# Optimization experiments

Hardware: AMD Instinct MI355X
Metric: run time of the kernel (lower is better)

## Reference

```python
import jax, jax.numpy as jnp
import numpy as np

N_NODES = 100000
N_EDGES = 1600000
IN_CH = 128
HEADS = 4
OUT_CH = 32


def setup_inputs() -> dict:
    key = jax.random.key(0)
    k = jax.random.split(key, 6)
    x = jax.random.normal(k[0], (N_NODES, IN_CH), dtype=jnp.float32)
    edge_index = jax.random.randint(k[1], (2, N_EDGES), 0, N_NODES, dtype=jnp.int64)
    edge_weight = jax.random.uniform(k[2], (N_EDGES,), dtype=jnp.float32)
    # torch Linear weight layout: (out_features, in_features) = (heads*out_ch, in_ch)
    W = jax.random.normal(k[3], (HEADS * OUT_CH, IN_CH), dtype=jnp.float32) * (1.0 / np.sqrt(IN_CH))
    a_src = jax.random.normal(k[4], (1, HEADS, OUT_CH), dtype=jnp.float32) * 0.1
    a_dst = jax.random.normal(k[5], (1, HEADS, OUT_CH), dtype=jnp.float32) * 0.1
    return {"x": x, "edge_index": edge_index, "edge_weight": edge_weight,
            "W": W, "a_src": a_src, "a_dst": a_dst}


def reference(x, edge_index, edge_weight, W, a_src, a_dst):
    N = x.shape[0]
    H, C = a_src.shape[1], a_src.shape[2]
    # linear projection then reshape to (N, H, C)
    h = (x @ W.T).reshape(N, H, C)
    src, dst = edge_index[0], edge_index[1]
    # per-node attention logits (node-level, then gathered -> same math as
    # (h[src]*a_src).sum(-1), computed once per node instead of per edge)
    s_src = jnp.sum(h * a_src, axis=-1)  # (N, H)
    s_dst = jnp.sum(h * a_dst, axis=-1)  # (N, H)
    alpha = jax.nn.leaky_relu(s_src[src] + s_dst[dst], negative_slope=0.2)  # (E, H)
    alpha = alpha * edge_weight[:, None]
    # segment softmax over dst; torch scatter_reduce amax with include_self=True
    # includes the zero init, so max is taken vs. 0 via zeros init
    amax = jnp.zeros((N, H), dtype=alpha.dtype).at[dst].max(alpha)
    alpha = jnp.exp(alpha - amax[dst])
    asum = jnp.zeros((N, H), dtype=alpha.dtype).at[dst].add(alpha)
    alpha = alpha / (asum[dst] + 1e-8)  # (E, H)
    # weighted scatter-add aggregation
    out = jnp.zeros((N, H, C), dtype=h.dtype).at[dst].add(h[src] * alpha[:, :, None])
    # concat=True
    return out.reshape(N, H * C)
```

## Files before the change

### kernel.cpp

```cpp
#include <hip/hip_runtime.h>

#define N_NODES 100000
#define N_EDGES 1600000
#define NBKT 391
#define BKT_SLACK 5120
#define EPB 4096
#define BINA_BLOCKS ((N_EDGES + EPB - 1) / EPB)

typedef __attribute__((ext_vector_type(8))) short short8;
typedef __attribute__((ext_vector_type(4))) float f32x4;

__device__ __forceinline__ unsigned short f2bf(float f) {
    unsigned u = __float_as_uint(f);
    u = u + 0x7fffu + ((u >> 16) & 1u);
    return (unsigned short)(u >> 16);
}
__device__ __forceinline__ float bf2f(unsigned short h) {
    return __uint_as_float((unsigned)h << 16);
}

__global__ __launch_bounds__(256) void proj_kernel(
    const float* __restrict__ x, const float* __restrict__ W,
    const float* __restrict__ a_src, const float* __restrict__ a_dst,
    unsigned short* __restrict__ hout, float* __restrict__ s_src,
    float* __restrict__ s_dst)
{
    __shared__ char smem[16384];
    char* xh = smem;
    char* xl = smem + 8192;
    const int t = threadIdx.x;
    const int br = blockIdx.x * 32;
    const int wave = t >> 6, lane = t & 63;
    const int lr = lane & 15, q = lane >> 4;

    short8 wh[2][4], wl[2][4];
#pragma unroll
    for (int ct = 0; ct < 2; ++ct) {
#pragma unroll
        for (int ks = 0; ks < 4; ++ks) {
            int o = wave * 32 + ct * 16 + lr;
            int k0 = (ks * 4 + q) * 8;
            float4 v0 = *(const float4*)&W[o * 128 + k0];
            float4 v1 = *(const float4*)&W[o * 128 + k0 + 4];
            float vv[8] = {v0.x, v0.y, v0.z, v0.w, v1.x, v1.y, v1.z, v1.w};
            short8 h8, l8;
#pragma unroll
            for (int j = 0; j < 8; ++j) {
                unsigned short hi = f2bf(vv[j]);
                h8[j] = (short)hi;
                l8[j] = (short)f2bf(vv[j] - bf2f(hi));
            }
            wh[ct][ks] = h8;
            wl[ct][ks] = l8;
        }
    }

    {
        int row = t >> 3;
        size_t gb = (size_t)(br + row) * 128;
#pragma unroll
        for (int i = 0; i < 4; ++i) {
            int k = ((t & 7) * 4 + i) * 4;
            float4 v = *(const float4*)&x[gb + k];
            ushort4 hi, lo;
            hi.x = f2bf(v.x); lo.x = f2bf(v.x - bf2f(hi.x));
            hi.y = f2bf(v.y); lo.y = f2bf(v.y - bf2f(hi.y));
            hi.z = f2bf(v.z); lo.z = f2bf(v.z - bf2f(hi.z));
            hi.w = f2bf(v.w); lo.w = f2bf(v.w - bf2f(hi.w));
            int byt = row * 256 + (((k >> 3) ^ (row & 7)) * 16) + (k & 7) * 2;
            *(ushort4*)(xh + byt) = hi;
            *(ushort4*)(xl + byt) = lo;
        }
    }
    __syncthreads();

    f32x4 acc[2][2] = {};

#pragma unroll
    for (int ks = 0; ks < 4; ++ks) {
        int sl = ((ks * 4 + q) ^ (lr & 7)) * 16;
        int a0o = lr * 256 + sl, a1o = (16 + lr) * 256 + sl;
        short8 ah0 = *(const short8*)(xh + a0o);
        short8 ah1 = *(const short8*)(xh + a1o);
        short8 al0 = *(const short8*)(xl + a0o);
        short8 al1 = *(const short8*)(xl + a1o);
        acc[0][0] = __builtin_amdgcn_mfma_f32_16x16x32_bf16(ah0, wh[0][ks], acc[0][0], 0, 0, 0);
        acc[0][1] = __builtin_amdgcn_mfma_f32_16x16x32_bf16(ah0, wh[1][ks], acc[0][1], 0, 0, 0);
        acc[1][0] = __builtin_amdgcn_mfma_f32_16x16x32_bf16(ah1, wh[0][ks], acc[1][0], 0, 0, 0);
        acc[1][1] = __builtin_amdgcn_mfma_f32_16x16x32_bf16(ah1, wh[1][ks], acc[1][1], 0, 0, 0);
        acc[0][0] = __builtin_amdgcn_mfma_f32_16x16x32_bf16(al0, wh[0][ks], acc[0][0], 0, 0, 0);
        acc[0][1] = __builtin_amdgcn_mfma_f32_16x16x32_bf16(al0, wh[1][ks], acc[0][1], 0, 0, 0);
        acc[1][0] = __builtin_amdgcn_mfma_f32_16x16x32_bf16(al1, wh[0][ks], acc[1][0], 0, 0, 0);
        acc[1][1] = __builtin_amdgcn_mfma_f32_16x16x32_bf16(al1, wh[1][ks], acc[1][1], 0, 0, 0);
        acc[0][0] = __builtin_amdgcn_mfma_f32_16x16x32_bf16(ah0, wl[0][ks], acc[0][0], 0, 0, 0);
        acc[0][1] = __builtin_amdgcn_mfma_f32_16x16x32_bf16(ah0, wl[1][ks], acc[0][1], 0, 0, 0);
        acc[1][0] = __builtin_amdgcn_mfma_f32_16x16x32_bf16(ah1, wl[0][ks], acc[1][0], 0, 0, 0);
        acc[1][1] = __builtin_amdgcn_mfma_f32_16x16x32_bf16(ah1, wl[1][ks], acc[1][1], 0, 0, 0);
    }

    float as0 = a_src[wave * 32 + lr], as1 = a_src[wave * 32 + 16 + lr];
    float ad0 = a_dst[wave * 32 + lr], ad1 = a_dst[wave * 32 + 16 + lr];
#pragma unroll
    for (int r = 0; r < 2; ++r) {
#pragma unroll
        for (int reg = 0; reg < 4; ++reg) {
            float ps = acc[r][0][reg] * as0 + acc[r][1][reg] * as1;
            float pd = acc[r][0][reg] * ad0 + acc[r][1][reg] * ad1;
            ps += __shfl_xor(ps, 1); ps += __shfl_xor(ps, 2);
            ps += __shfl_xor(ps, 4); ps += __shfl_xor(ps, 8);
            pd += __shfl_xor(pd, 1); pd += __shfl_xor(pd, 2);
            pd += __shfl_xor(pd, 4); pd += __shfl_xor(pd, 8);
            if (lr == 0) {
                int grow = br + r * 16 + q * 4 + reg;
                s_src[grow * 4 + wave] = ps;
                s_dst[grow * 4 + wave] = pd;
            }
        }
    }

    __syncthreads();
    unsigned short* hl = (unsigned short*)smem;
#pragma unroll
    for (int r = 0; r < 2; ++r)
#pragma unroll
        for (int c = 0; c < 2; ++c)
#pragma unroll
            for (int reg = 0; reg < 4; ++reg)
                hl[(r * 16 + q * 4 + reg) * 128 + wave * 32 + c * 16 + lr] =
                    f2bf(acc[r][c][reg]);
    __syncthreads();
    {
        int row = t >> 3, cb = (t & 7) * 16;
        uint4 v0 = *(uint4*)&hl[row * 128 + cb];
        uint4 v1 = *(uint4*)&hl[row * 128 + cb + 8];
        *(uint4*)&hout[(size_t)(br + row) * 128 + cb] = v0;
        *(uint4*)&hout[(size_t)(br + row) * 128 + cb + 8] = v1;
    }
}

__global__ __launch_bounds__(256) void binA_kernel(
    const int* __restrict__ ei, const float* __restrict__ ew,
    int* __restrict__ gcur, uint2* __restrict__ ebin)
{
    __shared__ int hist[NBKT];
    __shared__ int runbase[NBKT];
    const int t = threadIdx.x;
    const int base = blockIdx.x * EPB;
    for (int b = t; b < NBKT; b += 256) hist[b] = 0;
    __syncthreads();
#pragma unroll
    for (int i = 0; i < EPB / 256; ++i) {
        int e = base + i * 256 + t;
        if (e < N_EDGES) atomicAdd(&hist[ei[N_EDGES + e] >> 8], 1);
    }
    __syncthreads();
    for (int b = t; b < NBKT; b += 256) {
        int c = hist[b];
        runbase[b] = (c > 0) ? atomicAdd(&gcur[b], c) : 0;
        hist[b] = 0;
    }
    __syncthreads();
#pragma unroll
    for (int i = 0; i < EPB / 256; ++i) {
        int e = base + i * 256 + t;
        if (e >= N_EDGES) continue;
        int s = ei[e];
        int d = ei[N_EDGES + e];
        int b = d >> 8;
        int lpos = atomicAdd(&hist[b], 1);
        ebin[(size_t)b * BKT_SLACK + runbase[b] + lpos] =
            make_uint2((unsigned)s | ((unsigned)(d & 255) << 17),
                       __float_as_uint(ew[e]));
    }
}

__global__ __launch_bounds__(256) void binB_kernel(
    const uint2* __restrict__ ebin, const int* __restrict__ gcur,
    uint2* __restrict__ earr, int* __restrict__ rowp, int* __restrict__ deg)
{
    __shared__ int cnt[256];
    __shared__ int sc[256];
    __shared__ int cur[256];
    const int b = blockIdx.x;
    const int t = threadIdx.x;
    int acc = 0;
    for (int i = t; i < b; i += 256) acc += gcur[i];
    sc[t] = acc; __syncthreads();
    for (int off = 1; off < 256; off <<= 1) {
        int a = sc[t];
        int bb = (t >= off) ? sc[t - off] : 0;
        __syncthreads();
        sc[t] = a + bb;
        __syncthreads();
    }
    const int base = sc[255];
    __syncthreads();
    cnt[t] = 0;
    __syncthreads();
    const int count = gcur[b];
    const uint2* bp = ebin + (size_t)b * BKT_SLACK;
    for (int i = t; i < count; i += 256)
        atomicAdd(&cnt[(bp[i].x >> 17) & 255], 1);
    __syncthreads();
    int c = cnt[t];
    sc[t] = c; __syncthreads();
    for (int off = 1; off < 256; off <<= 1) {
        int a = sc[t];
        int bb = (t >= off) ? sc[t - off] : 0;
        __syncthreads();
        sc[t] = a + bb;
        __syncthreads();
    }
    int excl = sc[t] - c;
    int node = b * 256 + t;
    if (node < N_NODES) { rowp[node] = base + excl; deg[node] = c; }
    cur[t] = base + excl;
    __syncthreads();
    for (int i = t; i < count; i += 256) {
        uint2 rec = bp[i];
        int pos = atomicAdd(&cur[(rec.x >> 17) & 255], 1);
        earr[pos] = make_uint2(rec.x & 0x1FFFFu, rec.y);
    }
}

__global__ __launch_bounds__(256) void gather_kernel(
    const uint2* __restrict__ earr, const int* __restrict__ rowp,
    const int* __restrict__ deg, const float* __restrict__ s_src,
    const float* __restrict__ s_dst,
    const unsigned short* __restrict__ hbuf, float* __restrict__ out)
{
    __shared__ float lds_alpha[16][17][4];
    __shared__ int lds_src[16][17];
    const int ln = threadIdx.x >> 4;
    const int sub = threadIdx.x & 15;
    const int n = blockIdx.x * 16 + ln;
    const int start = rowp[n];
    const int dg = deg[n];
    const float4 sd = *(const float4*)&s_dst[n * 4];
    const int hd3 = sub >> 2;

    float ps0 = 0.f, ps1 = 0.f, ps2 = 0.f, ps3 = 0.f;
    float ac0 = 0.f, ac1 = 0.f, ac2 = 0.f, ac3 = 0.f;
    float ac4 = 0.f, ac5 = 0.f, ac6 = 0.f, ac7 = 0.f;

    for (int b0 = 0; b0 < dg; b0 += 16) {
        int nb = dg - b0; if (nb > 16) nb = 16;
        float a0 = 0.f, a1 = 0.f, a2 = 0.f, a3 = 0.f;
        int sid = 0;
        if (sub < nb) {
            uint2 rec = earr[start + b0 + sub];
            sid = (int)rec.x;
            float wgt = __uint_as_float(rec.y);
            float4 ss = *(const float4*)&s_src[sid * 4];
            float v;
            v = ss.x + sd.x; v = (v > 0.f ? v : 0.2f * v) * wgt; a0 = __expf(v);
            v = ss.y + sd.y; v = (v > 0.f ? v : 0.2f * v) * wgt; a1 = __expf(v);
            v = ss.z + sd.z; v = (v > 0.f ? v : 0.2f * v) * wgt; a2 = __expf(v);
            v = ss.w + sd.w; v = (v > 0.f ? v : 0.2f * v) * wgt; a3 = __expf(v);
            ps0 += a0; ps1 += a1; ps2 += a2; ps3 += a3;
        }
        *(float4*)&lds_alpha[ln][sub][0] = make_float4(a0, a1, a2, a3);
        lds_src[ln][sub] = sid;

        float co[16];
        uint4 hv[16];
#pragma unroll
        for (int e = 0; e < 16; ++e) {
            co[e] = lds_alpha[ln][e][hd3];
            int s = lds_src[ln][e];
            hv[e] = *(const uint4*)&hbuf[(size_t)s * 128 + sub * 8];
        }
#pragma unroll
        for (int e = 0; e < 16; ++e) {
            ac0 = fmaf(co[e], __uint_as_float(hv[e].x << 16), ac0);
            ac1 = fmaf(co[e], __uint_as_float(hv[e].x & 0xffff0000u), ac1);
            ac2 = fmaf(co[e], __uint_as_float(hv[e].y << 16), ac2);
            ac3 = fmaf(co[e], __uint_as_float(hv[e].y & 0xffff0000u), ac3);
            ac4 = fmaf(co[e], __uint_as_float(hv[e].z << 16), ac4);
            ac5 = fmaf(co[e], __uint_as_float(hv[e].z & 0xffff0000u), ac5);
            ac6 = fmaf(co[e], __uint_as_float(hv[e].w << 16), ac6);
            ac7 = fmaf(co[e], __uint_as_float(hv[e].w & 0xffff0000u), ac7);
        }
    }
#pragma unroll
    for (int off = 1; off < 16; off <<= 1) {
        ps0 += __shfl_xor(ps0, off);
        ps1 += __shfl_xor(ps1, off);
        ps2 += __shfl_xor(ps2, off);
        ps3 += __shfl_xor(ps3, off);
    }
    float sv = (hd3 & 2) ? ((hd3 & 1) ? ps3 : ps2) : ((hd3 & 1) ? ps1 : ps0);
    float inv = 1.f / (sv + 1e-8f);
    float4 o0 = {ac0 * inv, ac1 * inv, ac2 * inv, ac3 * inv};
    float4 o1 = {ac4 * inv, ac5 * inv, ac6 * inv, ac7 * inv};
    *(float4*)&out[(size_t)n * 128 + sub * 8] = o0;
    *(float4*)&out[(size_t)n * 128 + sub * 8 + 4] = o1;
}

extern "C" void kernel_launch(void* const* d_in, const int* in_sizes, int n_in,
                              void* d_out, int out_size, void* d_ws, size_t ws_size,
                              hipStream_t stream)
{
    const float* x     = (const float*)d_in[0];
    const int*   ei    = (const int*)d_in[1];
    const float* ew    = (const float*)d_in[2];
    const float* W     = (const float*)d_in[3];
    const float* a_src = (const float*)d_in[4];
    const float* a_dst = (const float*)d_in[5];
    float* out = (float*)d_out;
    char* ws = (char*)d_ws;

    unsigned short* hbuf = (unsigned short*)(ws);
    float* s_src = (float*)(ws + 25600000);
    float* s_dst = (float*)(ws + 27200000);
    int*   deg   = (int*)(ws + 28800000);
    int*   rowp  = (int*)(ws + 29200000);
    int*   gcur  = (int*)(ws + 29600000);
    uint2* earr  = (uint2*)(ws + 29669632);
    uint2* ebin  = (uint2*)(ws + 42469632);

    hipMemsetAsync(gcur, 0, 2048, stream);

    proj_kernel<<<N_NODES / 32, 256, 0, stream>>>(x, W, a_src, a_dst,
                                                  hbuf, s_src, s_dst);
    binA_kernel<<<BINA_BLOCKS, 256, 0, stream>>>(ei, ew, gcur, ebin);
    binB_kernel<<<NBKT, 256, 0, stream>>>(ebin, gcur, earr, rowp, deg);
    gather_kernel<<<N_NODES / 16, 256, 0, stream>>>(earr, rowp, deg, s_src, s_dst,
                                                    hbuf, out);
}
```

Measured before the change: 166.0 us.

## Merge projection and edge binning into one launch, double projection rows per block

The projection and first edge-binning pass are combined into a single kernel whose grid is split by block index, so the two independent stages run concurrently and one launch is removed. Each projection block now handles 64 rows instead of 32, with bounds checks added for the tail. This amortizes the per-block W split into high and low bf16 halves over more rows. Shared memory grows to about 33KB for every block, including binning blocks that need far less, which may reduce occupancy.

```diff
diff --git a/kernel.cpp b/kernel.cpp
--- a/kernel.cpp
+++ b/kernel.cpp
@@ -6,6 +6,7 @@
 #define BKT_SLACK 5120
 #define EPB 4096
 #define BINA_BLOCKS ((N_EDGES + EPB - 1) / EPB)
+#define PROJ_BLOCKS ((N_NODES + 63) / 64)
 
 typedef __attribute__((ext_vector_type(8))) short short8;
 typedef __attribute__((ext_vector_type(4))) float f32x4;
@@ -19,17 +20,53 @@
     return __uint_as_float((unsigned)h << 16);
 }
 
-__global__ __launch_bounds__(256) void proj_kernel(
+__global__ __launch_bounds__(256) void projbinA_kernel(
     const float* __restrict__ x, const float* __restrict__ W,
     const float* __restrict__ a_src, const float* __restrict__ a_dst,
     unsigned short* __restrict__ hout, float* __restrict__ s_src,
-    float* __restrict__ s_dst)
+    float* __restrict__ s_dst,
+    const int* __restrict__ ei, const float* __restrict__ ew,
+    int* __restrict__ gcur, uint2* __restrict__ ebin)
 {
-    __shared__ char smem[16384];
+    __shared__ char smem[33024];
+    const int t = threadIdx.x;
+
+    if (blockIdx.x >= PROJ_BLOCKS) {
+        int* hist    = (int*)smem;
+        int* runbase = (int*)(smem + 1664);
+        const int base = (blockIdx.x - PROJ_BLOCKS) * EPB;
+        for (int b = t; b < NBKT; b += 256) hist[b] = 0;
+        __syncthreads();
+#pragma unroll
+        for (int i = 0; i < EPB / 256; ++i) {
+            int e = base + i * 256 + t;
+            if (e < N_EDGES) atomicAdd(&hist[ei[N_EDGES + e] >> 8], 1);
+        }
+        __syncthreads();
+        for (int b = t; b < NBKT; b += 256) {
+            int c = hist[b];
+            runbase[b] = (c > 0) ? atomicAdd(&gcur[b], c) : 0;
+            hist[b] = 0;
+        }
+        __syncthreads();
+#pragma unroll
+        for (int i = 0; i < EPB / 256; ++i) {
+            int e = base + i * 256 + t;
+            if (e >= N_EDGES) continue;
+            int s = ei[e];
+            int d = ei[N_EDGES + e];
+            int b = d >> 8;
+            int lpos = atomicAdd(&hist[b], 1);
+            ebin[(size_t)b * BKT_SLACK + runbase[b] + lpos] =
+                make_uint2((unsigned)s | ((unsigned)(d & 255) << 17),
+                           __float_as_uint(ew[e]));
+        }
+        return;
+    }
+
     char* xh = smem;
-    char* xl = smem + 8192;
-    const int t = threadIdx.x;
-    const int br = blockIdx.x * 32;
+    char* xl = smem + 16384;
+    const int br = blockIdx.x * 64;
     const int wave = t >> 6, lane = t & 63;
     const int lr = lane & 15, q = lane >> 4;
 
@@ -56,12 +93,14 @@
     }
 
     {
-        int row = t >> 3;
-        size_t gb = (size_t)(br + row) * 128;
-#pragma unroll
-        for (int i = 0; i < 4; ++i) {
-            int k = ((t & 7) * 4 + i) * 4;
-            float4 v = *(const float4*)&x[gb + k];
+        int row = t >> 2;
+        int gr = br + row;
+        size_t gb = (size_t)gr * 128;
+#pragma unroll
+        for (int i = 0; i < 8; ++i) {
+            int k = (t & 3) * 32 + i * 4;
+            float4 v = (gr < N_NODES) ? *(const float4*)&x[gb + k]
+                                      : make_float4(0.f, 0.f, 0.f, 0.f);
             ushort4 hi, lo;
             hi.x = f2bf(v.x); lo.x = f2bf(v.x - bf2f(hi.x));
             hi.y = f2bf(v.y); lo.y = f2bf(v.y - bf2f(hi.y));
@@ -74,34 +113,29 @@
     }
     __syncthreads();
 
-    f32x4 acc[2][2] = {};
+    f32x4 acc[4][2] = {};
 
 #pragma unroll
     for (int ks = 0; ks < 4; ++ks) {
         int sl = ((ks * 4 + q) ^ (lr & 7)) * 16;
-        int a0o = lr * 256 + sl, a1o = (16 + lr) * 256 + sl;
-        short8 ah0 = *(const short8*)(xh + a0o);
-        short8 ah1 = *(const short8*)(xh + a1o);
-        short8 al0 = *(const short8*)(xl + a0o);
-        short8 al1 = *(const short8*)(xl + a1o);
-        acc[0][0] = __builtin_amdgcn_mfma_f32_16x16x32_bf16(ah0, wh[0][ks], acc[0][0], 0, 0, 0);
-        acc[0][1] = __builtin_amdgcn_mfma_f32_16x16x32_bf16(ah0, wh[1][ks], acc[0][1], 0, 0, 0);
-        acc[1][0] = __builtin_amdgcn_mfma_f32_16x16x32_bf16(ah1, wh[0][ks], acc[1][0], 0, 0, 0);
-        acc[1][1] = __builtin_amdgcn_mfma_f32_16x16x32_bf16(ah1, wh[1][ks], acc[1][1], 0, 0, 0);
-        acc[0][0] = __builtin_amdgcn_mfma_f32_16x16x32_bf16(al0, wh[0][ks], acc[0][0], 0, 0, 0);
-        acc[0][1] = __builtin_amdgcn_mfma_f32_16x16x32_bf16(al0, wh[1][ks], acc[0][1], 0, 0, 0);
-        acc[1][0] = __builtin_amdgcn_mfma_f32_16x16x32_bf16(al1, wh[0][ks], acc[1][0], 0, 0, 0);
-        acc[1][1] = __builtin_amdgcn_mfma_f32_16x16x32_bf16(al1, wh[1][ks], acc[1][1], 0, 0, 0);
-        acc[0][0] = __builtin_amdgcn_mfma_f32_16x16x32_bf16(ah0, wl[0][ks], acc[0][0], 0, 0, 0);
-        acc[0][1] = __builtin_amdgcn_mfma_f32_16x16x32_bf16(ah0, wl[1][ks], acc[0][1], 0, 0, 0);
-        acc[1][0] = __builtin_amdgcn_mfma_f32_16x16x32_bf16(ah1, wl[0][ks], acc[1][0], 0, 0, 0);
-        acc[1][1] = __builtin_amdgcn_mfma_f32_16x16x32_bf16(ah1, wl[1][ks], acc[1][1], 0, 0, 0);
+#pragma unroll
+        for (int r = 0; r < 4; ++r) {
+            int ao = (r * 16 + lr) * 256 + sl;
+            short8 ah = *(const short8*)(xh + ao);
+            short8 al = *(const short8*)(xl + ao);
+            acc[r][0] = __builtin_amdgcn_mfma_f32_16x16x32_bf16(ah, wh[0][ks], acc[r][0], 0, 0, 0);
+            acc[r][1] = __builtin_amdgcn_mfma_f32_16x16x32_bf16(ah, wh[1][ks], acc[r][1], 0, 0, 0);
+            acc[r][0] = __builtin_amdgcn_mfma_f32_16x16x32_bf16(al, wh[0][ks], acc[r][0], 0, 0, 0);
+            acc[r][1] = __builtin_amdgcn_mfma_f32_16x16x32_bf16(al, wh[1][ks], acc[r][1], 0, 0, 0);
+            acc[r][0] = __builtin_amdgcn_mfma_f32_16x16x32_bf16(ah, wl[0][ks], acc[r][0], 0, 0, 0);
+            acc[r][1] = __builtin_amdgcn_mfma_f32_16x16x32_bf16(ah, wl[1][ks], acc[r][1], 0, 0, 0);
+        }
     }
 
     float as0 = a_src[wave * 32 + lr], as1 = a_src[wave * 32 + 16 + lr];
     float ad0 = a_dst[wave * 32 + lr], ad1 = a_dst[wave * 32 + 16 + lr];
 #pragma unroll
-    for (int r = 0; r < 2; ++r) {
+    for (int r = 0; r < 4; ++r) {
 #pragma unroll
         for (int reg = 0; reg < 4; ++reg) {
             float ps = acc[r][0][reg] * as0 + acc[r][1][reg] * as1;
@@ -112,8 +146,10 @@
             pd += __shfl_xor(pd, 4); pd += __shfl_xor(pd, 8);
             if (lr == 0) {
                 int grow = br + r * 16 + q * 4 + reg;
-                s_src[grow * 4 + wave] = ps;
-                s_dst[grow * 4 + wave] = pd;
+                if (grow < N_NODES) {
+                    s_src[grow * 4 + wave] = ps;
+                    s_dst[grow * 4 + wave] = pd;
+                }
             }
         }
     }
@@ -121,7 +157,7 @@
     __syncthreads();
     unsigned short* hl = (unsigned short*)smem;
 #pragma unroll
-    for (int r = 0; r < 2; ++r)
+    for (int r = 0; r < 4; ++r)
 #pragma unroll
         for (int c = 0; c < 2; ++c)
 #pragma unroll
@@ -130,47 +166,18 @@
                     f2bf(acc[r][c][reg]);
     __syncthreads();
     {
-        int row = t >> 3, cb = (t & 7) * 16;
-        uint4 v0 = *(uint4*)&hl[row * 128 + cb];
-        uint4 v1 = *(uint4*)&hl[row * 128 + cb + 8];
-        *(uint4*)&hout[(size_t)(br + row) * 128 + cb] = v0;
-        *(uint4*)&hout[(size_t)(br + row) * 128 + cb + 8] = v1;
-    }
-}
-
-__global__ __launch_bounds__(256) void binA_kernel(
-    const int* __restrict__ ei, const float* __restrict__ ew,
-    int* __restrict__ gcur, uint2* __restrict__ ebin)
-{
-    __shared__ int hist[NBKT];
-    __shared__ int runbase[NBKT];
-    const int t = threadIdx.x;
-    const int base = blockIdx.x * EPB;
-    for (int b = t; b < NBKT; b += 256) hist[b] = 0;
-    __syncthreads();
-#pragma unroll
-    for (int i = 0; i < EPB / 256; ++i) {
-        int e = base + i * 256 + t;
-        if (e < N_EDGES) atomicAdd(&hist[ei[N_EDGES + e] >> 8], 1);
-    }
-    __syncthreads();
-    for (int b = t; b < NBKT; b += 256) {
-        int c = hist[b];
-        runbase[b] = (c > 0) ? atomicAdd(&gcur[b], c) : 0;
-        hist[b] = 0;
-    }
-    __syncthreads();
-#pragma unroll
-    for (int i = 0; i < EPB / 256; ++i) {
-        int e = base + i * 256 + t;
-        if (e >= N_EDGES) continue;
-        int s = ei[e];
-        int d = ei[N_EDGES + e];
-        int b = d >> 8;
-        int lpos = atomicAdd(&hist[b], 1);
-        ebin[(size_t)b * BKT_SLACK + runbase[b] + lpos] =
-            make_uint2((unsigned)s | ((unsigned)(d & 255) << 17),
-                       __float_as_uint(ew[e]));
+        int row = t >> 2, cb = (t & 3) * 32;
+        int gr = br + row;
+        if (gr < N_NODES) {
+            uint4 v0 = *(uint4*)&hl[row * 128 + cb];
+            uint4 v1 = *(uint4*)&hl[row * 128 + cb + 8];
+            uint4 v2 = *(uint4*)&hl[row * 128 + cb + 16];
+            uint4 v3 = *(uint4*)&hl[row * 128 + cb + 24];
+            *(uint4*)&hout[(size_t)gr * 128 + cb] = v0;
+            *(uint4*)&hout[(size_t)gr * 128 + cb + 8] = v1;
+            *(uint4*)&hout[(size_t)gr * 128 + cb + 16] = v2;
+            *(uint4*)&hout[(size_t)gr * 128 + cb + 24] = v3;
+        }
     }
 }
 
@@ -321,9 +328,8 @@
 
     hipMemsetAsync(gcur, 0, 2048, stream);
 
-    proj_kernel<<<N_NODES / 32, 256, 0, stream>>>(x, W, a_src, a_dst,
-                                                  hbuf, s_src, s_dst);
-    binA_kernel<<<BINA_BLOCKS, 256, 0, stream>>>(ei, ew, gcur, ebin);
+    projbinA_kernel<<<PROJ_BLOCKS + BINA_BLOCKS, 256, 0, stream>>>(
+        x, W, a_src, a_dst, hbuf, s_src, s_dst, ei, ew, gcur, ebin);
     binB_kernel<<<NBKT, 256, 0, stream>>>(ebin, gcur, earr, rowp, deg);
     gather_kernel<<<N_NODES / 16, 256, 0, stream>>>(earr, rowp, deg, s_src, s_dst,
                                                     hbuf, out);
```

Measured after the change: 169.5 us. +2.1%, slower.
